# Optimization experiments

Hardware: AMD Instinct MI355X
Metric: run time of the kernel (lower is better)

Reference implementation:

```python
import jax, jax.numpy as jnp
import numpy as np

HEADS = 16
DIM_HEAD = 64
RMS_EPS = 1e-12  # torch F.normalize default eps


def setup_inputs() -> dict:
    key = jax.random.key(0)
    k1, k2, k3 = jax.random.split(key, 3)
    b, n, dim = 2, 2048, 1024
    dim_inner = HEADS * DIM_HEAD
    x = jax.random.normal(k1, (b, n, dim), dtype=jnp.float32)
    gamma = jnp.ones((dim,), dtype=jnp.float32)
    w_qkv = jax.random.normal(k2, (dim, 3 * dim_inner), dtype=jnp.float32) * (dim ** -0.5)
    w_out = jax.random.normal(k3, (dim_inner, dim), dtype=jnp.float32) * (dim_inner ** -0.5)
    return {"x": x, "gamma": gamma, "w_qkv": w_qkv, "w_out": w_out}


def reference(x, gamma, w_qkv, w_out):
    b, n, dim = x.shape
    h, d = HEADS, DIM_HEAD
    # RMSNorm: F.normalize(x, dim=-1) * sqrt(dim) * gamma
    l2 = jnp.maximum(jnp.linalg.norm(x, axis=-1, keepdims=True), RMS_EPS)
    normed = x / l2 * (dim ** 0.5) * gamma
    # qkv projection, split order: (qkv h d)
    qkv = (normed @ w_qkv).reshape(b, n, 3, h, d)
    qkv = jnp.transpose(qkv, (2, 0, 3, 1, 4))  # [3, b, h, n, d]
    q, k, v = qkv[0], qkv[1], qkv[2]
    q = q * (d ** -0.5)
    sim = jnp.einsum('bhid,bhjd->bhij', q, k)  # [b,h,n,n]
    mask_value = -jnp.finfo(sim.dtype).max
    causal_mask = jnp.triu(jnp.ones((n, n), dtype=bool), k=1)
    sim = jnp.where(causal_mask, mask_value, sim)
    attn = jax.nn.softmax(sim, axis=-1)
    out = jnp.einsum('bhij,bhjd->bhid', attn, v)  # [b,h,n,d]
    out = jnp.transpose(out, (0, 2, 1, 3)).reshape(b, n, h * d)
    return out @ w_out
```

## Files before the change

kernel.cpp:

```cpp
#include <hip/hip_runtime.h>
#include <hip/hip_bf16.h>

#define BATCH 2
#define SEQ 2048
#define DMODEL 1024
#define NHEAD 16
#define DHEAD 64
#define NQKV 3072
#define DINNER 1024

typedef __attribute__((ext_vector_type(4))) short short4v;
typedef __attribute__((ext_vector_type(8))) short short8v;
typedef __attribute__((ext_vector_type(4))) float f32x4;

__device__ __forceinline__ unsigned short f2bf(float f) {
  union { float f; unsigned int u; } c; c.f = f;
  unsigned int u = c.u;
  u += 0x7fffu + ((u >> 16) & 1u);
  return (unsigned short)(u >> 16);
}

__device__ __forceinline__ float exp2_hw(float x) {
  float r;
  asm("v_exp_f32 %0, %1" : "=v"(r) : "v"(x));
  return r;
}

#define GL16(gp, lp)                                             \
  __builtin_amdgcn_global_load_lds(                              \
      (__attribute__((address_space(1))) void*)(gp),             \
      (__attribute__((address_space(3))) void*)(lp), 16, 0, 0)

__global__ __launch_bounds__(256) void transpose_cast_kernel(const float* __restrict__ in,
                                                             unsigned short* __restrict__ out,
                                                             int K, int N) {
  __shared__ float tile[32][33];
  const int tiles_n = N >> 5;
  const int tn = blockIdx.x % tiles_n;
  const int tk = blockIdx.x / tiles_n;
  const int k0 = tk << 5, n0 = tn << 5;
  const int t = threadIdx.x;
#pragma unroll
  for (int p = 0; p < 4; p++) {
    const int e = p * 256 + t;
    const int r = e >> 5, c = e & 31;
    tile[r][c] = in[(size_t)(k0 + r) * N + n0 + c];
  }
  __syncthreads();
#pragma unroll
  for (int p = 0; p < 4; p++) {
    const int e = p * 256 + t;
    const int r = e >> 5, c = e & 31;
    out[(size_t)(n0 + r) * K + k0 + c] = f2bf(tile[c][r]);
  }
}

__global__ __launch_bounds__(256) void rmsnorm_kernel(const float* __restrict__ x,
                                                      const float* __restrict__ gamma,
                                                      unsigned short* __restrict__ out) {
  const int row = blockIdx.x;
  const int t = threadIdx.x;
  const float* xr = x + (size_t)row * DMODEL;
  float4 v = ((const float4*)xr)[t];
  float ss = v.x * v.x + v.y * v.y + v.z * v.z + v.w * v.w;
#pragma unroll
  for (int off = 1; off < 64; off <<= 1) ss += __shfl_xor(ss, off);
  __shared__ float wss[4];
  if ((t & 63) == 0) wss[t >> 6] = ss;
  __syncthreads();
  const float tot = wss[0] + wss[1] + wss[2] + wss[3];
  float l2 = sqrtf(tot);
  l2 = fmaxf(l2, 1e-12f);
  const float s = 32.0f / l2;
  const float4 gm = ((const float4*)gamma)[t];
  unsigned short o[4];
  o[0] = f2bf(v.x * s * gm.x);
  o[1] = f2bf(v.y * s * gm.y);
  o[2] = f2bf(v.z * s * gm.z);
  o[3] = f2bf(v.w * s * gm.w);
  unsigned short* op = out + (size_t)row * DMODEL + t * 4;
  *(short4v*)op = *(short4v*)o;
}

#define BM 128
#define BN 128
#define BKT 32
#define TILE_E (BM * BKT)

__device__ void gemm_core(const unsigned short* __restrict__ A,
                          const unsigned short* __restrict__ Bt, int K, int rowBase,
                          int colBase, unsigned short* sA, unsigned short* sB,
                          f32x4 acc[4][4]) {
  const int t = threadIdx.x;
  const int lane = t & 63, wave = t >> 6;
  const int l15 = lane & 15, g = lane >> 4;
  const int wr = (wave >> 1) * 64, wc = (wave & 1) * 64;
#pragma unroll
  for (int m = 0; m < 4; m++)
#pragma unroll
    for (int n = 0; n < 4; n++) acc[m][n] = (f32x4){0.f, 0.f, 0.f, 0.f};
  const int r0 = t >> 2, o0 = (t & 3) * 8;
  const unsigned short* Ag0 = A + (size_t)(rowBase + r0) * K + o0;
  const unsigned short* Ag1 = A + (size_t)(rowBase + r0 + 64) * K + o0;
  const unsigned short* Bg0 = Bt + (size_t)(colBase + r0) * K + o0;
  const unsigned short* Bg1 = Bt + (size_t)(colBase + r0 + 64) * K + o0;
  GL16(Ag0, sA + t * 8);
  GL16(Ag1, sA + (t + 256) * 8);
  GL16(Bg0, sB + t * 8);
  GL16(Bg1, sB + (t + 256) * 8);
  __syncthreads();
  int cur = 0;
  for (int k0 = 0; k0 < K; k0 += BKT, cur ^= 1) {
    if (k0 + BKT < K) {
      const int nxto = (cur ^ 1) * TILE_E;
      GL16(Ag0 + k0 + BKT, sA + nxto + t * 8);
      GL16(Ag1 + k0 + BKT, sA + nxto + (t + 256) * 8);
      GL16(Bg0 + k0 + BKT, sB + nxto + t * 8);
      GL16(Bg1 + k0 + BKT, sB + nxto + (t + 256) * 8);
    }
    const unsigned short* sAc = sA + cur * TILE_E;
    const unsigned short* sBc = sB + cur * TILE_E;
    short8v af[4], bf[4];
#pragma unroll
    for (int m = 0; m < 4; m++)
      af[m] = *(const short8v*)(sAc + (wr + m * 16 + l15) * BKT + 8 * g);
#pragma unroll
    for (int n = 0; n < 4; n++)
      bf[n] = *(const short8v*)(sBc + (wc + n * 16 + l15) * BKT + 8 * g);
#pragma unroll
    for (int m = 0; m < 4; m++)
#pragma unroll
      for (int n = 0; n < 4; n++)
        acc[m][n] = __builtin_amdgcn_mfma_f32_16x16x32_bf16(af[m], bf[n], acc[m][n], 0, 0, 0);
    __syncthreads();
  }
}

#define QBM 256
#define QBN 256
#define QBK 32
#define QTE (QBM * QBK)
#define QNT (DMODEL / QBK)

__global__ __launch_bounds__(512, 2) void qkv_gemm_kernel(const unsigned short* __restrict__ A,
                                                          const unsigned short* __restrict__ Bt,
                                                          unsigned short* __restrict__ qb,
                                                          unsigned short* __restrict__ kb,
                                                          unsigned short* __restrict__ vtb) {
  __shared__ __align__(16) unsigned short sA[3][QTE];
  __shared__ __align__(16) unsigned short sB[3][QTE];
  const int t = threadIdx.x, lane = t & 63, wave = t >> 6;
  const int l15 = lane & 15, g = lane >> 4;
  const int wm = wave >> 2, wn = wave & 3;
  const int nbn = NQKV / QBN;
  const int bm = blockIdx.x / nbn, bn = blockIdx.x % nbn;
  const int rowBase = bm * QBM, colBase = bn * QBN;
  const int r0 = t >> 2, j0 = t & 3;
  const int r1 = r0 + 128;
  const unsigned short* Ag0 = A + (size_t)(rowBase + r0) * DMODEL + ((j0 ^ (r0 & 3)) * 8);
  const unsigned short* Ag1 = A + (size_t)(rowBase + r1) * DMODEL + ((j0 ^ (r1 & 3)) * 8);
  const unsigned short* Bg0 = Bt + (size_t)(colBase + r0) * DMODEL + ((j0 ^ (r0 & 3)) * 8);
  const unsigned short* Bg1 = Bt + (size_t)(colBase + r1) * DMODEL + ((j0 ^ (r1 & 3)) * 8);

  f32x4 acc[8][4];
#pragma unroll
  for (int mi = 0; mi < 8; mi++)
#pragma unroll
    for (int ni = 0; ni < 4; ni++) acc[mi][ni] = (f32x4){0.f, 0.f, 0.f, 0.f};

#pragma unroll
  for (int tt = 0; tt < 2; ++tt) {
    GL16(Ag0 + tt * QBK, sA[tt] + t * 8);
    GL16(Ag1 + tt * QBK, sA[tt] + (t + 512) * 8);
    GL16(Bg0 + tt * QBK, sB[tt] + t * 8);
    GL16(Bg1 + tt * QBK, sB[tt] + (t + 512) * 8);
  }
  asm volatile("s_waitcnt vmcnt(4)" ::: "memory");
  __builtin_amdgcn_sched_barrier(0);
  __builtin_amdgcn_s_barrier();

  for (int kt = 0; kt < QNT; ++kt) {
    const unsigned short* sAc = sA[kt % 3];
    const unsigned short* sBc = sB[kt % 3];
    const bool pf = (kt + 2 < QNT);
    const int nb = (kt + 2) % 3;
    const int ko = (kt + 2) * QBK;
    short8v af[8], bf[4];
#pragma unroll
    for (int mi = 0; mi < 4; mi++) {
      const int row = wm * 128 + mi * 16 + l15;
      af[mi] = *(const short8v*)(sAc + row * QBK + ((g ^ (row & 3)) * 8));
    }
#pragma unroll
    for (int ni = 0; ni < 4; ni++) {
      const int row = wn * 64 + ni * 16 + l15;
      bf[ni] = *(const short8v*)(sBc + row * QBK + ((g ^ (row & 3)) * 8));
    }
    if (pf) {
      GL16(Ag0 + ko, sA[nb] + t * 8);
      GL16(Ag1 + ko, sA[nb] + (t + 512) * 8);
    }
    asm volatile("s_waitcnt lgkmcnt(0)" ::: "memory");
    __builtin_amdgcn_sched_barrier(0);
    __builtin_amdgcn_s_setprio(1);
#pragma unroll
    for (int mi = 0; mi < 4; mi++)
#pragma unroll
      for (int ni = 0; ni < 4; ni++)
        acc[mi][ni] = __builtin_amdgcn_mfma_f32_16x16x32_bf16(af[mi], bf[ni], acc[mi][ni], 0, 0, 0);
    __builtin_amdgcn_s_setprio(0);
#pragma unroll
    for (int mi = 4; mi < 8; mi++) {
      const int row = wm * 128 + mi * 16 + l15;
      af[mi] = *(const short8v*)(sAc + row * QBK + ((g ^ (row & 3)) * 8));
    }
    if (pf) {
      GL16(Bg0 + ko, sB[nb] + t * 8);
      GL16(Bg1 + ko, sB[nb] + (t + 512) * 8);
    }
    asm volatile("s_waitcnt lgkmcnt(0)" ::: "memory");
    __builtin_amdgcn_sched_barrier(0);
    __builtin_amdgcn_s_setprio(1);
#pragma unroll
    for (int mi = 4; mi < 8; mi++)
#pragma unroll
      for (int ni = 0; ni < 4; ni++)
        acc[mi][ni] = __builtin_amdgcn_mfma_f32_16x16x32_bf16(af[mi], bf[ni], acc[mi][ni], 0, 0, 0);
    __builtin_amdgcn_s_setprio(0);
    if (pf) asm volatile("s_waitcnt vmcnt(4)" ::: "memory");
    else    asm volatile("s_waitcnt vmcnt(0)" ::: "memory");
    __builtin_amdgcn_sched_barrier(0);
    __builtin_amdgcn_s_barrier();
  }

#pragma unroll
  for (int mi = 0; mi < 8; mi++)
#pragma unroll
    for (int ni = 0; ni < 4; ni++) {
      const int col = colBase + wn * 64 + ni * 16 + l15;
      const int part = col >> 10;
      const int h = (col >> 6) & 15;
      const int d = col & 63;
      const int row0 = rowBase + wm * 128 + mi * 16 + 4 * g;
      const int bb = row0 >> 11, i0 = row0 & 2047;
      if (part == 2) {
        const int ip = (i0 & ~31) | (((i0 >> 2) & 3) << 3) | (((i0 >> 4) & 1) << 2);
        union { short4v v; unsigned short u[4]; } pk;
#pragma unroll
        for (int r = 0; r < 4; r++) pk.u[r] = f2bf(acc[mi][ni][r]);
        *(short4v*)(vtb + ((size_t)(bb * NHEAD + h) * DHEAD + d) * SEQ + ip) = pk.v;
      } else {
#pragma unroll
        for (int r = 0; r < 4; r++) {
          const size_t idx = (((size_t)(bb * NHEAD + h)) * SEQ + i0 + r) * DHEAD + d;
          const float v = acc[mi][ni][r];
          if (part == 0) qb[idx] = f2bf(v * 0.18033688f);
          else kb[idx] = f2bf(v);
        }
      }
    }
}

__global__ __launch_bounds__(256) void out_gemm_kernel(const unsigned short* __restrict__ A,
                                                       const unsigned short* __restrict__ Bt,
                                                       float* __restrict__ C) {
  __shared__ __align__(16) unsigned short sA[2 * TILE_E];
  __shared__ __align__(16) unsigned short sB[2 * TILE_E];
  const int nbn = DMODEL / BN;
  const int bm = blockIdx.x / nbn, bn = blockIdx.x % nbn;
  f32x4 acc[4][4];
  gemm_core(A, Bt, DINNER, bm * BM, bn * BN, sA, sB, acc);
  const int t = threadIdx.x, lane = t & 63, wave = t >> 6;
  const int l15 = lane & 15, g = lane >> 4;
  const int wr = (wave >> 1) * 64, wc = (wave & 1) * 64;
#pragma unroll
  for (int m = 0; m < 4; m++)
#pragma unroll
    for (int n = 0; n < 4; n++) {
      const int col = bn * BN + wc + n * 16 + l15;
#pragma unroll
      for (int r = 0; r < 4; r++) {
        const int row = bm * BM + wr + m * 16 + 4 * g + r;
        C[(size_t)row * DMODEL + col] = acc[m][n][r];
      }
    }
}

__global__ __launch_bounds__(256, 4) void attn_kernel(const unsigned short* __restrict__ qb,
                                                      const unsigned short* __restrict__ kb,
                                                      const unsigned short* __restrict__ vtb,
                                                      unsigned short* __restrict__ ob) {
  __shared__ __align__(16) unsigned short sK[2][64 * 64];
  __shared__ __align__(16) unsigned short sV[2][64 * 72];
  const int t = threadIdx.x, lane = t & 63, wave = t >> 6;
  const int l15 = lane & 15, g = lane >> 4;
  const int bh = blockIdx.x & 31;
  const int qord = blockIdx.x >> 5;
  const int qblk = (qord < 8) ? 31 - qord
                 : (qord < 16) ? qord - 8
                 : (qord < 24) ? 39 - qord
                 : qord - 16;
  const int qrow = qblk * 64 + wave * 16 + l15;
  const unsigned short* qptr = qb + (size_t)bh * SEQ * DHEAD;
  const unsigned short* kptr = kb + (size_t)bh * SEQ * DHEAD;
  const unsigned short* vtptr = vtb + (size_t)bh * DHEAD * SEQ;

  const int kr0 = t >> 3, kj0 = ((t & 7) ^ (kr0 & 7)) * 8;
  const int kr1 = (t + 256) >> 3, kj1 = ((t & 7) ^ (kr1 & 7)) * 8;
  const int vr0 = t >> 3, vo0 = (t & 7) * 8;
  const int vr1 = (t + 256) >> 3, vo1 = (t & 7) * 8;

  short8v qf[2];
#pragma unroll
  for (int kk = 0; kk < 2; kk++)
    qf[kk] = *(const short8v*)(qptr + (size_t)qrow * DHEAD + kk * 32 + 8 * g);

  union { short8v v; unsigned short u[8]; } ones;
#pragma unroll
  for (int j = 0; j < 8; j++) ones.u[j] = 0x3F80;

  float rm = -__builtin_inff();
  f32x4 acc_l = (f32x4){0.f, 0.f, 0.f, 0.f};
  f32x4 acc_o[4];
#pragma unroll
  for (int df = 0; df < 4; df++) acc_o[df] = (f32x4){0.f, 0.f, 0.f, 0.f};

  const int nsteps = qblk + 1;

  GL16(kptr + (size_t)kr0 * DHEAD + kj0, sK[0] + t * 8);
  GL16(kptr + (size_t)kr1 * DHEAD + kj1, sK[0] + (t + 256) * 8);
  {
    short8v va = *(const short8v*)(vtptr + (size_t)vr0 * SEQ + vo0);
    short8v vb = *(const short8v*)(vtptr + (size_t)vr1 * SEQ + vo1);
    *(short8v*)(sV[0] + vr0 * 72 + vo0) = va;
    *(short8v*)(sV[0] + vr1 * 72 + vo1) = vb;
  }
  __syncthreads();

  int cur = 0;
  for (int s = 0; s < nsteps; ++s, cur ^= 1) {
    const int nxt = cur ^ 1;
    const bool more = (s + 1 < nsteps);
    short8v va, vb;
    if (more) {
      const int k0n = (s + 1) * 64;
      GL16(kptr + (size_t)(k0n + kr0) * DHEAD + kj0, sK[nxt] + t * 8);
      GL16(kptr + (size_t)(k0n + kr1) * DHEAD + kj1, sK[nxt] + (t + 256) * 8);
      va = *(const short8v*)(vtptr + (size_t)vr0 * SEQ + k0n + vo0);
      vb = *(const short8v*)(vtptr + (size_t)vr1 * SEQ + k0n + vo1);
    }
    {
      const int k0 = s * 64;
      const unsigned short* sKc = sK[cur];
      const unsigned short* sVc = sV[cur];
      short8v kf[4][2];
#pragma unroll
      for (int n4 = 0; n4 < 4; n4++) {
        const int row = n4 * 16 + l15;
#pragma unroll
        for (int kk = 0; kk < 2; kk++)
          kf[n4][kk] = *(const short8v*)(sKc + row * 64 + (((kk * 4 + g) ^ (row & 7)) * 8));
      }
      f32x4 s4[4];
#pragma unroll
      for (int n4 = 0; n4 < 4; n4++) s4[n4] = (f32x4){0.f, 0.f, 0.f, 0.f};
#pragma unroll
      for (int n4 = 0; n4 < 4; n4++)
#pragma unroll
        for (int kk = 0; kk < 2; kk++)
          s4[n4] = __builtin_amdgcn_mfma_f32_16x16x32_bf16(kf[n4][kk], qf[kk],
                                                           s4[n4], 0, 0, 0);
      if (s == nsteps - 1) {
#pragma unroll
        for (int n4 = 0; n4 < 4; n4++)
#pragma unroll
          for (int r = 0; r < 4; r++)
            if (k0 + n4 * 16 + 4 * g + r > qrow) s4[n4][r] = -__builtin_inff();
      }
      float mx = s4[0][0];
#pragma unroll
      for (int n4 = 0; n4 < 4; n4++)
#pragma unroll
        for (int r = 0; r < 4; r++)
          if (n4 || r) mx = fmaxf(mx, s4[n4][r]);
      if (!__all(mx <= rm)) {
        mx = fmaxf(mx, __shfl_xor(mx, 16));
        mx = fmaxf(mx, __shfl_xor(mx, 32));
        const float nm = fmaxf(rm, mx);
        const float al = exp2_hw(rm - nm);
        rm = nm;
#pragma unroll
        for (int r = 0; r < 4; r++) acc_l[r] *= al;
#pragma unroll
        for (int df = 0; df < 4; df++)
#pragma unroll
          for (int r = 0; r < 4; r++) acc_o[df][r] *= al;
      }
#pragma unroll
      for (int n4 = 0; n4 < 4; n4++)
#pragma unroll
        for (int r = 0; r < 4; r++) s4[n4][r] = exp2_hw(s4[n4][r] - rm);
      unsigned int pw[8];
#pragma unroll
      for (int n4 = 0; n4 < 4; n4++) {
        asm("v_cvt_pk_bf16_f32 %0, %1, %2"
            : "=v"(pw[n4 * 2]) : "v"(s4[n4][0]), "v"(s4[n4][1]));
        asm("v_cvt_pk_bf16_f32 %0, %1, %2"
            : "=v"(pw[n4 * 2 + 1]) : "v"(s4[n4][2]), "v"(s4[n4][3]));
      }
      union { short8v v; unsigned int wd[4]; } paA, paB;
      paA.wd[0] = pw[0]; paA.wd[1] = pw[1]; paA.wd[2] = pw[2]; paA.wd[3] = pw[3];
      paB.wd[0] = pw[4]; paB.wd[1] = pw[5]; paB.wd[2] = pw[6]; paB.wd[3] = pw[7];
      acc_l = __builtin_amdgcn_mfma_f32_16x16x32_bf16(ones.v, paA.v, acc_l, 0, 0, 0);
      acc_l = __builtin_amdgcn_mfma_f32_16x16x32_bf16(ones.v, paB.v, acc_l, 0, 0, 0);
#pragma unroll
      for (int df = 0; df < 4; df++) {
        const unsigned short* pv = sVc + (df * 16 + l15) * 72 + 8 * g;
        const short8v vfa = *(const short8v*)(pv);
        acc_o[df] = __builtin_amdgcn_mfma_f32_16x16x32_bf16(vfa, paA.v, acc_o[df], 0, 0, 0);
        const short8v vfb = *(const short8v*)(pv + 32);
        acc_o[df] = __builtin_amdgcn_mfma_f32_16x16x32_bf16(vfb, paB.v, acc_o[df], 0, 0, 0);
      }
    }
    if (more) {
      *(short8v*)(sV[nxt] + vr0 * 72 + vo0) = va;
      *(short8v*)(sV[nxt] + vr1 * 72 + vo1) = vb;
    }
    __syncthreads();
  }

  const int bb = bh >> 4, hh = bh & 15;
  const float inv = 1.0f / acc_l[0];
#pragma unroll
  for (int df = 0; df < 4; df++) {
    union { short4v v; unsigned short u[4]; } pk4;
#pragma unroll
    for (int r = 0; r < 4; r++) pk4.u[r] = f2bf(acc_o[df][r] * inv);
    *(short4v*)(ob + ((size_t)bb * SEQ + qrow) * DINNER + hh * DHEAD + df * 16 + 4 * g) =
        pk4.v;
  }
}

extern "C" void kernel_launch(void* const* d_in, const int* in_sizes, int n_in,
                              void* d_out, int out_size, void* d_ws, size_t ws_size,
                              hipStream_t stream) {
  (void)in_sizes; (void)n_in; (void)out_size; (void)ws_size;
  const float* x = (const float*)d_in[0];
  const float* gamma = (const float*)d_in[1];
  const float* w_qkv = (const float*)d_in[2];
  const float* w_out = (const float*)d_in[3];
  float* out = (float*)d_out;
  char* ws = (char*)d_ws;
  unsigned short* wqkvT = (unsigned short*)(ws);
  unsigned short* woutT = (unsigned short*)(ws + 6291456);
  unsigned short* normed = (unsigned short*)(ws + 8388608);
  unsigned short* qbuf = (unsigned short*)(ws + 16777216);
  unsigned short* kbuf = (unsigned short*)(ws + 25165824);
  unsigned short* vtbuf = (unsigned short*)(ws + 33554432);
  unsigned short* aout = (unsigned short*)(ws + 41943040);

  hipLaunchKernelGGL(transpose_cast_kernel, dim3((DMODEL / 32) * (NQKV / 32)), dim3(256), 0,
                     stream, w_qkv, wqkvT, DMODEL, NQKV);
  hipLaunchKernelGGL(transpose_cast_kernel, dim3((DINNER / 32) * (DMODEL / 32)), dim3(256), 0,
                     stream, w_out, woutT, DINNER, DMODEL);
  hipLaunchKernelGGL(rmsnorm_kernel, dim3(BATCH * SEQ), dim3(256), 0, stream, x, gamma, normed);
  hipLaunchKernelGGL(qkv_gemm_kernel, dim3((BATCH * SEQ / QBM) * (NQKV / QBN)), dim3(512), 0,
                     stream, normed, wqkvT, qbuf, kbuf, vtbuf);
  hipLaunchKernelGGL(attn_kernel, dim3(BATCH * NHEAD * 32), dim3(256), 0, stream,
                     qbuf, kbuf, vtbuf, aout);
  hipLaunchKernelGGL(out_gemm_kernel, dim3((BATCH * SEQ / BM) * (DMODEL / BN)), dim3(256), 0,
                     stream, aout, woutT, out);
}
```

Baseline: 112.0 us.

## Shrink QKV GEMM tiles to 128x64 and swizzle LDS in both GEMMs

The QKV projection GEMM moves from 256x256 tiles with 512 threads to 128x64 tiles with 256 threads, so the grid grows from 192 to 1536 blocks and fills the CUs better, at the cost of more global traffic per FLOP. The pipeline loop is simplified to a single MFMA phase per k-step. Both the QKV and output GEMMs now use a (row>>1)&3 XOR swizzle on the LDS layout to cut bank conflicts on the fragment reads; the output GEMM previously had no swizzle.

```diff
diff --git a/kernel.cpp b/kernel.cpp
--- a/kernel.cpp
+++ b/kernel.cpp
@@ -99,11 +99,12 @@
   for (int m = 0; m < 4; m++)
 #pragma unroll
     for (int n = 0; n < 4; n++) acc[m][n] = (f32x4){0.f, 0.f, 0.f, 0.f};
-  const int r0 = t >> 2, o0 = (t & 3) * 8;
-  const unsigned short* Ag0 = A + (size_t)(rowBase + r0) * K + o0;
-  const unsigned short* Ag1 = A + (size_t)(rowBase + r0 + 64) * K + o0;
-  const unsigned short* Bg0 = Bt + (size_t)(colBase + r0) * K + o0;
-  const unsigned short* Bg1 = Bt + (size_t)(colBase + r0 + 64) * K + o0;
+  const int r0 = t >> 2, j0 = t & 3;
+  const int swz = (r0 >> 1) & 3;
+  const unsigned short* Ag0 = A + (size_t)(rowBase + r0) * K + ((j0 ^ swz) * 8);
+  const unsigned short* Ag1 = A + (size_t)(rowBase + r0 + 64) * K + ((j0 ^ swz) * 8);
+  const unsigned short* Bg0 = Bt + (size_t)(colBase + r0) * K + ((j0 ^ swz) * 8);
+  const unsigned short* Bg1 = Bt + (size_t)(colBase + r0 + 64) * K + ((j0 ^ swz) * 8);
   GL16(Ag0, sA + t * 8);
   GL16(Ag1, sA + (t + 256) * 8);
   GL16(Bg0, sB + t * 8);
@@ -122,11 +123,15 @@
     const unsigned short* sBc = sB + cur * TILE_E;
     short8v af[4], bf[4];
 #pragma unroll
-    for (int m = 0; m < 4; m++)
-      af[m] = *(const short8v*)(sAc + (wr + m * 16 + l15) * BKT + 8 * g);
-#pragma unroll
-    for (int n = 0; n < 4; n++)
-      bf[n] = *(const short8v*)(sBc + (wc + n * 16 + l15) * BKT + 8 * g);
+    for (int m = 0; m < 4; m++) {
+      const int row = wr + m * 16 + l15;
+      af[m] = *(const short8v*)(sAc + row * BKT + ((g ^ ((row >> 1) & 3)) * 8));
+    }
+#pragma unroll
+    for (int n = 0; n < 4; n++) {
+      const int row = wc + n * 16 + l15;
+      bf[n] = *(const short8v*)(sBc + row * BKT + ((g ^ ((row >> 1) & 3)) * 8));
+    }
 #pragma unroll
     for (int m = 0; m < 4; m++)
 #pragma unroll
@@ -136,46 +141,45 @@
   }
 }
 
-#define QBM 256
-#define QBN 256
+#define QBM 128
+#define QBN 64
 #define QBK 32
-#define QTE (QBM * QBK)
+#define QAE (QBM * QBK)
+#define QBE (QBN * QBK)
 #define QNT (DMODEL / QBK)
 
-__global__ __launch_bounds__(512, 2) void qkv_gemm_kernel(const unsigned short* __restrict__ A,
+__global__ __launch_bounds__(256, 4) void qkv_gemm_kernel(const unsigned short* __restrict__ A,
                                                           const unsigned short* __restrict__ Bt,
                                                           unsigned short* __restrict__ qb,
                                                           unsigned short* __restrict__ kb,
                                                           unsigned short* __restrict__ vtb) {
-  __shared__ __align__(16) unsigned short sA[3][QTE];
-  __shared__ __align__(16) unsigned short sB[3][QTE];
+  __shared__ __align__(16) unsigned short sA[3][QAE];
+  __shared__ __align__(16) unsigned short sB[3][QBE];
   const int t = threadIdx.x, lane = t & 63, wave = t >> 6;
   const int l15 = lane & 15, g = lane >> 4;
-  const int wm = wave >> 2, wn = wave & 3;
+  const int wm = wave >> 1, wn = wave & 1;
   const int nbn = NQKV / QBN;
   const int bm = blockIdx.x / nbn, bn = blockIdx.x % nbn;
   const int rowBase = bm * QBM, colBase = bn * QBN;
   const int r0 = t >> 2, j0 = t & 3;
-  const int r1 = r0 + 128;
-  const unsigned short* Ag0 = A + (size_t)(rowBase + r0) * DMODEL + ((j0 ^ (r0 & 3)) * 8);
-  const unsigned short* Ag1 = A + (size_t)(rowBase + r1) * DMODEL + ((j0 ^ (r1 & 3)) * 8);
-  const unsigned short* Bg0 = Bt + (size_t)(colBase + r0) * DMODEL + ((j0 ^ (r0 & 3)) * 8);
-  const unsigned short* Bg1 = Bt + (size_t)(colBase + r1) * DMODEL + ((j0 ^ (r1 & 3)) * 8);
-
-  f32x4 acc[8][4];
-#pragma unroll
-  for (int mi = 0; mi < 8; mi++)
-#pragma unroll
-    for (int ni = 0; ni < 4; ni++) acc[mi][ni] = (f32x4){0.f, 0.f, 0.f, 0.f};
+  const int swz = (r0 >> 1) & 3;
+  const unsigned short* Ag0 = A + (size_t)(rowBase + r0) * DMODEL + ((j0 ^ swz) * 8);
+  const unsigned short* Ag1 = A + (size_t)(rowBase + r0 + 64) * DMODEL + ((j0 ^ swz) * 8);
+  const unsigned short* Bg0 = Bt + (size_t)(colBase + r0) * DMODEL + ((j0 ^ swz) * 8);
+
+  f32x4 acc[4][2];
+#pragma unroll
+  for (int mi = 0; mi < 4; mi++)
+#pragma unroll
+    for (int ni = 0; ni < 2; ni++) acc[mi][ni] = (f32x4){0.f, 0.f, 0.f, 0.f};
 
 #pragma unroll
   for (int tt = 0; tt < 2; ++tt) {
     GL16(Ag0 + tt * QBK, sA[tt] + t * 8);
-    GL16(Ag1 + tt * QBK, sA[tt] + (t + 512) * 8);
+    GL16(Ag1 + tt * QBK, sA[tt] + (t + 256) * 8);
     GL16(Bg0 + tt * QBK, sB[tt] + t * 8);
-    GL16(Bg1 + tt * QBK, sB[tt] + (t + 512) * 8);
-  }
-  asm volatile("s_waitcnt vmcnt(4)" ::: "memory");
+  }
+  asm volatile("s_waitcnt vmcnt(3)" ::: "memory");
   __builtin_amdgcn_sched_barrier(0);
   __builtin_amdgcn_s_barrier();
 
@@ -185,20 +189,21 @@
     const bool pf = (kt + 2 < QNT);
     const int nb = (kt + 2) % 3;
     const int ko = (kt + 2) * QBK;
-    short8v af[8], bf[4];
+    short8v af[4], bf[2];
 #pragma unroll
     for (int mi = 0; mi < 4; mi++) {
-      const int row = wm * 128 + mi * 16 + l15;
-      af[mi] = *(const short8v*)(sAc + row * QBK + ((g ^ (row & 3)) * 8));
-    }
-#pragma unroll
-    for (int ni = 0; ni < 4; ni++) {
-      const int row = wn * 64 + ni * 16 + l15;
-      bf[ni] = *(const short8v*)(sBc + row * QBK + ((g ^ (row & 3)) * 8));
+      const int row = wm * 64 + mi * 16 + l15;
+      af[mi] = *(const short8v*)(sAc + row * QBK + ((g ^ ((row >> 1) & 3)) * 8));
+    }
+#pragma unroll
+    for (int ni = 0; ni < 2; ni++) {
+      const int row = wn * 32 + ni * 16 + l15;
+      bf[ni] = *(const short8v*)(sBc + row * QBK + ((g ^ ((row >> 1) & 3)) * 8));
     }
     if (pf) {
       GL16(Ag0 + ko, sA[nb] + t * 8);
-      GL16(Ag1 + ko, sA[nb] + (t + 512) * 8);
+      GL16(Ag1 + ko, sA[nb] + (t + 256) * 8);
+      GL16(Bg0 + ko, sB[nb] + t * 8);
     }
     asm volatile("s_waitcnt lgkmcnt(0)" ::: "memory");
     __builtin_amdgcn_sched_barrier(0);
@@ -206,42 +211,24 @@
 #pragma unroll
     for (int mi = 0; mi < 4; mi++)
 #pragma unroll
-      for (int ni = 0; ni < 4; ni++)
+      for (int ni = 0; ni < 2; ni++)
         acc[mi][ni] = __builtin_amdgcn_mfma_f32_16x16x32_bf16(af[mi], bf[ni], acc[mi][ni], 0, 0, 0);
     __builtin_amdgcn_s_setprio(0);
-#pragma unroll
-    for (int mi = 4; mi < 8; mi++) {
-      const int row = wm * 128 + mi * 16 + l15;
-      af[mi] = *(const short8v*)(sAc + row * QBK + ((g ^ (row & 3)) * 8));
-    }
-    if (pf) {
-      GL16(Bg0 + ko, sB[nb] + t * 8);
-      GL16(Bg1 + ko, sB[nb] + (t + 512) * 8);
-    }
-    asm volatile("s_waitcnt lgkmcnt(0)" ::: "memory");
-    __builtin_amdgcn_sched_barrier(0);
-    __builtin_amdgcn_s_setprio(1);
-#pragma unroll
-    for (int mi = 4; mi < 8; mi++)
-#pragma unroll
-      for (int ni = 0; ni < 4; ni++)
-        acc[mi][ni] = __builtin_amdgcn_mfma_f32_16x16x32_bf16(af[mi], bf[ni], acc[mi][ni], 0, 0, 0);
-    __builtin_amdgcn_s_setprio(0);
-    if (pf) asm volatile("s_waitcnt vmcnt(4)" ::: "memory");
+    if (pf) asm volatile("s_waitcnt vmcnt(3)" ::: "memory");
     else    asm volatile("s_waitcnt vmcnt(0)" ::: "memory");
     __builtin_amdgcn_sched_barrier(0);
     __builtin_amdgcn_s_barrier();
   }
 
 #pragma unroll
-  for (int mi = 0; mi < 8; mi++)
-#pragma unroll
-    for (int ni = 0; ni < 4; ni++) {
-      const int col = colBase + wn * 64 + ni * 16 + l15;
+  for (int mi = 0; mi < 4; mi++)
+#pragma unroll
+    for (int ni = 0; ni < 2; ni++) {
+      const int col = colBase + wn * 32 + ni * 16 + l15;
       const int part = col >> 10;
       const int h = (col >> 6) & 15;
       const int d = col & 63;
-      const int row0 = rowBase + wm * 128 + mi * 16 + 4 * g;
+      const int row0 = rowBase + wm * 64 + mi * 16 + 4 * g;
       const int bb = row0 >> 11, i0 = row0 & 2047;
       if (part == 2) {
         const int ip = (i0 & ~31) | (((i0 >> 2) & 3) << 3) | (((i0 >> 4) & 1) << 2);
@@ -464,7 +451,7 @@
   hipLaunchKernelGGL(transpose_cast_kernel, dim3((DINNER / 32) * (DMODEL / 32)), dim3(256), 0,
                      stream, w_out, woutT, DINNER, DMODEL);
   hipLaunchKernelGGL(rmsnorm_kernel, dim3(BATCH * SEQ), dim3(256), 0, stream, x, gamma, normed);
-  hipLaunchKernelGGL(qkv_gemm_kernel, dim3((BATCH * SEQ / QBM) * (NQKV / QBN)), dim3(512), 0,
+  hipLaunchKernelGGL(qkv_gemm_kernel, dim3((BATCH * SEQ / QBM) * (NQKV / QBN)), dim3(256), 0,
                      stream, normed, wqkvT, qbuf, kbuf, vtbuf);
   hipLaunchKernelGGL(attn_kernel, dim3(BATCH * NHEAD * 32), dim3(256), 0, stream,
                      qbuf, kbuf, vtbuf, aout);
```

After: 118.2 us. 5.6% more time.
